# Kernel tuning notes

Hardware: AMD Instinct MI355X
Metric: run time of the kernel (lower is better)

## Reference

```python
import jax, jax.numpy as jnp
import numpy as np

NK, NV, DK, DV = 16, 32, 128, 128
R = NV // NK
KCONV, CHUNK = 4, 64
KEY_DIM, VALUE_DIM = NK * DK, NV * DV
CONV_DIM = 2 * KEY_DIM + VALUE_DIM
HIDDEN = 2048
B, S = 1, 4096


def _l2norm(x, eps=1e-6):
    return x * jax.lax.rsqrt(jnp.sum(x * x, -1, keepdims=True) + eps)


def _causal_dwconv(x, w):
    # x: [B, C, S], w: [C, K]; depthwise causal conv (pad K-1 on left),
    # equivalent to torch F.conv1d(groups=C, padding=K-1)[..., :S]
    K = w.shape[-1]
    T = x.shape[-1]
    xp = jnp.pad(x, ((0, 0), (0, 0), (K - 1, 0)))
    out = jnp.zeros_like(x)
    for j in range(K):  # fixed tiny kernel taps
        out = out + w[None, :, j, None] * xp[:, :, j:j + T]
    return out


def _chunk_gated_delta_rule(q, k, v, g, beta):
    # q,k: [B,S,H,DK], v: [B,S,H,DV], g,beta: [B,S,H]; S % CHUNK == 0
    dtype0 = q.dtype
    q = _l2norm(q)
    k = _l2norm(k)
    tr = lambda x: jnp.swapaxes(x, 1, 2).astype(jnp.float32)
    q, k, v = tr(q), tr(k), tr(v)
    g = jnp.swapaxes(g, 1, 2).astype(jnp.float32)
    beta = jnp.swapaxes(beta, 1, 2).astype(jnp.float32)
    Bb, H, T, dk = k.shape
    dv = v.shape[-1]
    N = T // CHUNK
    q = q * dk ** -0.5
    v_beta = v * beta[..., None]
    k_beta = k * beta[..., None]
    resh = lambda x: x.reshape(Bb, H, N, CHUNK, x.shape[-1])
    q, k, v, k_beta, v_beta = map(resh, (q, k, v, k_beta, v_beta))
    g = jnp.cumsum(g.reshape(Bb, H, N, CHUNK), axis=-1)
    lo = jnp.tril(jnp.ones((CHUNK, CHUNK), bool))
    lo_strict = jnp.tril(jnp.ones((CHUNK, CHUNK), bool), -1)
    gdiff = g[..., :, None] - g[..., None, :]
    decay = jnp.where(lo, jnp.exp(jnp.where(lo, gdiff, 0.0)), 0.0)  # [B,H,N,C,C]
    # strictly-lower M = tril_{-1}(k_beta @ k^T * decay); the original in-chunk
    # forward-substitution loop computes exactly (I + M)^{-1}
    M = jnp.where(lo_strict, jnp.einsum('bhnik,bhnjk->bhnij', k_beta, k) * decay, 0.0)
    eye = jnp.eye(CHUNK, dtype=jnp.float32)
    T_inv = jax.scipy.linalg.solve_triangular(
        eye + M, jnp.broadcast_to(eye, M.shape), lower=True, unit_diagonal=True)
    v_c = jnp.einsum('bhnij,bhnjv->bhniv', T_inv, v_beta)
    k_cumdecay = jnp.einsum('bhnij,bhnjk->bhnik', T_inv, k_beta * jnp.exp(g)[..., None])
    attn_local = jnp.where(lo, jnp.einsum('bhnik,bhnjk->bhnij', q, k) * decay, 0.0)
    mv = lambda x: jnp.moveaxis(x, 2, 0)  # chunk axis to front for scan
    xs = (mv(q), mv(k), mv(v_c), mv(g), mv(attn_local), mv(k_cumdecay))
    S0 = jnp.zeros((Bb, H, dk, dv), jnp.float32)

    def step(state, inp):
        q_i, k_i, v_i, g_i, attn_i, kcd_i = inp
        g_last = g_i[..., -1]  # [B,H]
        v_prime = jnp.einsum('bhik,bhkv->bhiv', kcd_i, state)
        v_new = v_i - v_prime
        attn_inter = jnp.einsum('bhik,bhkv->bhiv', q_i * jnp.exp(g_i)[..., None], state)
        out_i = attn_inter + jnp.einsum('bhij,bhjv->bhiv', attn_i, v_new)
        k_dec = k_i * jnp.exp(g_last[..., None] - g_i)[..., None]
        new_state = state * jnp.exp(g_last)[..., None, None] + \
            jnp.einsum('bhik,bhiv->bhkv', k_dec, v_new)
        return new_state, out_i

    _, outs = jax.lax.scan(step, S0, xs)  # [N,B,H,C,DV]
    core = jnp.moveaxis(outs, 0, 2).reshape(Bb, H, T, dv)
    return jnp.swapaxes(core, 1, 2).astype(dtype0)


def _forward(hidden_states, W_qkvz, W_ba, conv_w, dt_bias, A_log, norm_weight, W_out):
    Bx, Sx, _ = hidden_states.shape
    qkvz = (hidden_states @ W_qkvz).reshape(Bx, Sx, NK, 2 * DK + 2 * R * DV)
    ba = (hidden_states @ W_ba).reshape(Bx, Sx, NK, 2 * R)
    q = qkvz[..., :DK]
    k = qkvz[..., DK:2 * DK]
    v = qkvz[..., 2 * DK:2 * DK + R * DV].reshape(Bx, Sx, NV, DV)
    z = qkvz[..., 2 * DK + R * DV:].reshape(Bx, Sx, NV, DV)
    b = ba[..., :R].reshape(Bx, Sx, NV)
    a = ba[..., R:].reshape(Bx, Sx, NV)
    mixed = jnp.concatenate(
        [q.reshape(Bx, Sx, -1), k.reshape(Bx, Sx, -1), v.reshape(Bx, Sx, -1)], axis=-1)
    mixed = jax.nn.silu(_causal_dwconv(jnp.swapaxes(mixed, 1, 2), conv_w))
    mixed = jnp.swapaxes(mixed, 1, 2)
    q = mixed[..., :KEY_DIM].reshape(Bx, Sx, NK, DK)
    k = mixed[..., KEY_DIM:2 * KEY_DIM].reshape(Bx, Sx, NK, DK)
    v = mixed[..., 2 * KEY_DIM:].reshape(Bx, Sx, NV, DV)
    beta = jax.nn.sigmoid(b)
    g = -jnp.exp(A_log.astype(jnp.float32)) * jax.nn.softplus(
        a.astype(jnp.float32) + dt_bias.astype(jnp.float32))
    q = jnp.repeat(q, R, axis=2)  # GQA: expand k-heads to v-heads
    k = jnp.repeat(k, R, axis=2)
    core = _chunk_gated_delta_rule(q, k, v, g, beta)  # [B,S,NV,DV]
    h = core.astype(jnp.float32)
    h = h * jax.lax.rsqrt(jnp.mean(h * h, axis=-1, keepdims=True) + 1e-6)
    h = norm_weight * h
    h = h * jax.nn.silu(z.astype(jnp.float32))
    return h.reshape(Bx, Sx, VALUE_DIM) @ W_out


def setup_inputs() -> dict:
    ks = jax.random.split(jax.random.key(0), 8)
    return {
        'hidden_states': jax.random.normal(ks[0], (B, S, HIDDEN), jnp.float32),
        'W_qkvz': jax.random.normal(ks[1], (HIDDEN, 2 * KEY_DIM + 2 * VALUE_DIM), jnp.float32) * 0.02,
        'W_ba': jax.random.normal(ks[2], (HIDDEN, 2 * NV), jnp.float32) * 0.02,
        'conv_w': jax.random.normal(ks[3], (CONV_DIM, KCONV), jnp.float32) * 0.2,
        'dt_bias': jax.random.normal(ks[4], (NV,), jnp.float32) * 0.1,
        'A_log': jax.random.normal(ks[5], (NV,), jnp.float32) * 0.1,
        'norm_weight': jnp.ones((DV,), jnp.float32),
        'W_out': jax.random.normal(ks[6], (VALUE_DIM, HIDDEN), jnp.float32) * 0.02,
    }


def reference(hidden_states, W_qkvz, W_ba, conv_w, dt_bias, A_log, norm_weight, W_out):
    return _forward(hidden_states, W_qkvz, W_ba, conv_w, dt_bias, A_log, norm_weight, W_out)
```

## Files before the change

kernel.cpp:

```cpp
#include <hip/hip_runtime.h>

typedef unsigned short u16;
typedef __attribute__((ext_vector_type(2))) float f32x2;
typedef __attribute__((ext_vector_type(4))) float f32x4;
typedef __attribute__((ext_vector_type(2))) u16 u16x2;
typedef __attribute__((ext_vector_type(4))) u16 u16x4;
typedef __attribute__((ext_vector_type(8))) u16 u16x8;
typedef __attribute__((ext_vector_type(8))) __bf16 bf16x8;

__device__ __forceinline__ float bf2f(u16 u){ unsigned v = ((unsigned)u) << 16; return __builtin_bit_cast(float, v); }
__device__ __forceinline__ u16 f2bf(float f){
  unsigned u = __builtin_bit_cast(unsigned, f);
  u += 0x7fffu + ((u >> 16) & 1u);
  return (u16)(u >> 16);
}
__device__ __forceinline__ f32x4 b4f(u16x4 u){
  f32x4 r; r[0] = bf2f(u[0]); r[1] = bf2f(u[1]); r[2] = bf2f(u[2]); r[3] = bf2f(u[3]); return r;
}
__device__ __forceinline__ u16x4 p4(f32x4 v){
  u16x4 o; o[0] = f2bf(v[0]); o[1] = f2bf(v[1]); o[2] = f2bf(v[2]); o[3] = f2bf(v[3]); return o;
}
__device__ __forceinline__ void gld16(const void* g, const void* l){
  __builtin_amdgcn_global_load_lds((__attribute__((address_space(1))) void*)(void*)g,
                                   (__attribute__((address_space(3))) void*)(void*)l, 16, 0, 0);
}
__device__ __forceinline__ float sigmoidf(float x){ return 1.f / (1.f + expf(-x)); }
__device__ __forceinline__ float siluf(float x){ return x / (1.f + expf(-x)); }

#define GBAR() do { asm volatile("" ::: "memory"); __builtin_amdgcn_s_barrier(); asm volatile("" ::: "memory"); } while(0)

__global__ __launch_bounds__(256) void k_cast(const float* __restrict__ in, u16* __restrict__ out, int n4){
  int t = blockIdx.x * 256 + threadIdx.x;
  if (t >= n4) return;
  f32x4 v = ((const f32x4*)in)[t];
  u16x4 o;
  o[0] = f2bf(v[0]); o[1] = f2bf(v[1]); o[2] = f2bf(v[2]); o[3] = f2bf(v[3]);
  ((u16x4*)out)[t] = o;
}

template<int PERM>
__global__ __launch_bounds__(256) void k_trans(const float* __restrict__ in, u16* __restrict__ out, int K, int N){
  __shared__ float tile[32][33];
  int tx = threadIdx.x, ty = threadIdx.y;
  int n0 = blockIdx.x * 32, k0 = blockIdx.y * 32;
  #pragma unroll
  for (int j = 0; j < 32; j += 8) tile[ty + j][tx] = in[(size_t)(k0 + ty + j) * N + n0 + tx];
  __syncthreads();
  #pragma unroll
  for (int j = 0; j < 32; j += 8){
    int n = n0 + ty + j;
    int np;
    if (PERM){
      int g = n / 768, r = n - g * 768;
      np = (r < 512) ? (g * 512 + r) : (8192 + g * 256 + (r - 512));
    } else np = n;
    out[(size_t)np * K + k0 + tx] = f2bf(tile[tx][ty + j]);
  }
}

template<int MODE>
__global__ __launch_bounds__(512) void k_gemm256(const u16* __restrict__ A, const u16* __restrict__ Bt,
                                                 void* __restrict__ C, void* __restrict__ C2, int N, int K){
  __shared__ alignas(16) char lds[131072];
  const int tid = threadIdx.x;
  const int wid = tid >> 6, lane = tid & 63;
  const int vl = lane & 15, kg = lane >> 4;
  const int wm = wid >> 2, wn = wid & 3;
  const int nwg = (int)gridDim.x;
  const int swzb = ((int)blockIdx.x & 7) * (nwg >> 3) + ((int)blockIdx.x >> 3);
  const int nbx = N >> 8;
  const int bx = swzb % nbx, by = swzb / nbx;
  const int gm = by << 8, gn = bx << 8;
  const int nt = K >> 6;

  auto stageA = [&](int t, int h){
    if (t >= nt) return;
    const int k0 = t << 6;
    char* slot = lds + ((t & 1) * 2 + h) * 16384;
    #pragma unroll
    for (int p = 0; p < 2; p++){
      int o = p * 8192 + wid * 1024 + lane * 16;
      int sr = o >> 7, cs = (o >> 4) & 7;
      int gr = gm + ((sr >> 6) << 7) + h * 64 + (sr & 63);
      int gc = k0 + ((cs ^ (sr & 7)) << 3);
      gld16(A + (size_t)gr * K + gc, slot + p * 8192 + wid * 1024);
    }
  };
  auto stageB = [&](int t, int h){
    if (t >= nt) return;
    const int k0 = t << 6;
    char* slot = lds + 65536 + ((t & 1) * 2 + h) * 16384;
    #pragma unroll
    for (int p = 0; p < 2; p++){
      int o = p * 8192 + wid * 1024 + lane * 16;
      int sr = o >> 7, cs = (o >> 4) & 7;
      int gr = gn + ((sr >> 5) << 6) + h * 32 + (sr & 31);
      int gc = k0 + ((cs ^ (sr & 7)) << 3);
      gld16(Bt + (size_t)gr * K + gc, slot + p * 8192 + wid * 1024);
    }
  };

  f32x4 acc[8][4];
  #pragma unroll
  for (int a = 0; a < 8; a++)
    #pragma unroll
    for (int b = 0; b < 4; b++) acc[a][b] = 0.f;

  stageA(0, 0); stageB(0, 0); stageA(0, 1); stageB(0, 1); stageA(1, 0); stageB(1, 0);
  asm volatile("s_waitcnt vmcnt(8)" ::: "memory");
  GBAR();

#define PHASE(MH, NH, STAGECALL, VMSEL) do { \
    const char* Asl_ = lds + ((cur * 2 + (MH)) * 16384); \
    const char* Bsl_ = lds + 65536 + ((cur * 2 + (NH)) * 16384); \
    bf16x8 af_[4][2], bf_[2][2]; \
    _Pragma("unroll") \
    for (int mi = 0; mi < 4; mi++){ \
      int sr = wm * 64 + mi * 16 + vl; \
      _Pragma("unroll") \
      for (int ks = 0; ks < 2; ks++) \
        af_[mi][ks] = __builtin_bit_cast(bf16x8, *(const u16x8*)(Asl_ + sr * 128 + (((ks * 4 + kg) ^ (vl & 7)) << 4))); \
    } \
    _Pragma("unroll") \
    for (int ni = 0; ni < 2; ni++){ \
      int br = wn * 32 + ni * 16 + vl; \
      _Pragma("unroll") \
      for (int ks = 0; ks < 2; ks++) \
        bf_[ni][ks] = __builtin_bit_cast(bf16x8, *(const u16x8*)(Bsl_ + br * 128 + (((ks * 4 + kg) ^ (vl & 7)) << 4))); \
    } \
    STAGECALL; \
    __builtin_amdgcn_s_setprio(1); \
    _Pragma("unroll") \
    for (int mi = 0; mi < 4; mi++) \
      _Pragma("unroll") \
      for (int ni = 0; ni < 2; ni++) \
        _Pragma("unroll") \
        for (int ks = 0; ks < 2; ks++) \
          acc[(MH) * 4 + mi][(NH) * 2 + ni] = __builtin_amdgcn_mfma_f32_16x16x32_bf16(af_[mi][ks], bf_[ni][ks], acc[(MH) * 4 + mi][(NH) * 2 + ni], 0, 0, 0); \
    __builtin_amdgcn_s_setprio(0); \
    VMSEL; \
    GBAR(); \
  } while (0)

  for (int t = 0; t < nt; t++){
    const int cur = t & 1;
    const bool tail = (t >= nt - 3);
    PHASE(0, 0, stageA(t + 1, 1),
          { if (!tail) asm volatile("s_waitcnt vmcnt(6)" ::: "memory");
            else       asm volatile("s_waitcnt vmcnt(0)" ::: "memory"); });
    PHASE(0, 1, stageB(t + 1, 1), {});
    PHASE(1, 0, stageA(t + 2, 0), {});
    PHASE(1, 1, stageB(t + 2, 0),
          { if (!tail) asm volatile("s_waitcnt vmcnt(8)" ::: "memory");
            else       asm volatile("s_waitcnt vmcnt(0)" ::: "memory"); });
  }
#undef PHASE

  #pragma unroll
  for (int a = 0; a < 8; a++){
    int row = gm + wm * 128 + (a >> 2) * 64 + (a & 3) * 16 + (lane >> 4) * 4;
    #pragma unroll
    for (int b = 0; b < 4; b++){
      int col = gn + wn * 64 + (b >> 1) * 32 + (b & 1) * 16 + vl;
      #pragma unroll
      for (int j = 0; j < 4; j++){
        if (MODE == 0){
          ((float*)C)[(size_t)(row + j) * N + col] = acc[a][b][j];
        } else {
          if (col < 8192) ((u16*)C)[(size_t)(row + j) * 8192 + col]         = f2bf(acc[a][b][j]);
          else            ((u16*)C2)[(size_t)(row + j) * 4096 + col - 8192] = f2bf(acc[a][b][j]);
        }
      }
    }
  }
}

template<int MODE>
__global__ __launch_bounds__(256) void k_gemm(const u16* __restrict__ A, const u16* __restrict__ Bt,
                                              void* __restrict__ C, void* __restrict__ C2, int N, int K){
  __shared__ u16 As[128 * 32];
  __shared__ u16 Bs[128 * 32];
  const int tid = threadIdx.x;
  const int wave = tid >> 6, lane = tid & 63;
  const int nbx = (int)gridDim.x;
  const int nwg = nbx * (int)gridDim.y;
  const int linear = (int)blockIdx.y * nbx + (int)blockIdx.x;
  const int swz = (linear & 7) * (nwg >> 3) + (linear >> 3);
  const int gm = (swz / nbx) * 128, gn = (swz % nbx) * 128;
  const int c0 = wave * 2, c1 = c0 + 1;
  const int r0 = c0 * 16 + (lane >> 2), r1 = r0 + 16;
  const int kp = (lane & 3) * 8;
  const u16* a0 = A + (size_t)(gm + r0) * K + kp;
  const u16* a1 = A + (size_t)(gm + r1) * K + kp;
  const u16* b0 = Bt + (size_t)(gn + r0) * K + kp;
  const u16* b1 = Bt + (size_t)(gn + r1) * K + kp;
  const int wr = (wave >> 1) * 64, wc = (wave & 1) * 64;
  f32x4 acc[4][4];
  #pragma unroll
  for (int m = 0; m < 4; m++)
    #pragma unroll
    for (int n = 0; n < 4; n++) acc[m][n] = 0.f;
  for (int k0 = 0; k0 < K; k0 += 32){
    __syncthreads();
    gld16(a0 + k0, &As[c0 * 512]);
    gld16(a1 + k0, &As[c1 * 512]);
    gld16(b0 + k0, &Bs[c0 * 512]);
    gld16(b1 + k0, &Bs[c1 * 512]);
    __syncthreads();
    bf16x8 af[4], bfv[4];
    #pragma unroll
    for (int m = 0; m < 4; m++)
      af[m] = __builtin_bit_cast(bf16x8, *(const u16x8*)&As[(wr + m * 16 + (lane & 15)) * 32 + (lane >> 4) * 8]);
    #pragma unroll
    for (int n = 0; n < 4; n++)
      bfv[n] = __builtin_bit_cast(bf16x8, *(const u16x8*)&Bs[(wc + n * 16 + (lane & 15)) * 32 + (lane >> 4) * 8]);
    #pragma unroll
    for (int m = 0; m < 4; m++)
      #pragma unroll
      for (int n = 0; n < 4; n++)
        acc[m][n] = __builtin_amdgcn_mfma_f32_16x16x32_bf16(af[m], bfv[n], acc[m][n], 0, 0, 0);
  }
  #pragma unroll
  for (int m = 0; m < 4; m++){
    int row = gm + wr + m * 16 + (lane >> 4) * 4;
    #pragma unroll
    for (int n = 0; n < 4; n++){
      int col = gn + wc + n * 16 + (lane & 15);
      #pragma unroll
      for (int j = 0; j < 4; j++){
        if (MODE == 0){
          ((float*)C)[(size_t)(row + j) * N + col] = acc[m][n][j];
        } else {
          if (col < 8192) ((u16*)C)[(size_t)(row + j) * 8192 + col]         = f2bf(acc[m][n][j]);
          else            ((u16*)C2)[(size_t)(row + j) * 4096 + col - 8192] = f2bf(acc[m][n][j]);
        }
      }
    }
  }
}

__global__ __launch_bounds__(256) void k_ba(const float* __restrict__ hs, const float* __restrict__ Wba,
                                            float* __restrict__ ba){
  int wave = threadIdx.x >> 6, lane = threadIdx.x & 63;
  int s0 = (blockIdx.x * 4 + wave) * 4;
  f32x4 acc = 0.f;
  for (int k = 0; k < 2048; k += 4){
    float w0 = Wba[(size_t)(k + 0) * 64 + lane];
    float w1 = Wba[(size_t)(k + 1) * 64 + lane];
    float w2 = Wba[(size_t)(k + 2) * 64 + lane];
    float w3 = Wba[(size_t)(k + 3) * 64 + lane];
    f32x4 h0 = *(const f32x4*)&hs[(size_t)(s0 + 0) * 2048 + k];
    f32x4 h1 = *(const f32x4*)&hs[(size_t)(s0 + 1) * 2048 + k];
    f32x4 h2 = *(const f32x4*)&hs[(size_t)(s0 + 2) * 2048 + k];
    f32x4 h3 = *(const f32x4*)&hs[(size_t)(s0 + 3) * 2048 + k];
    acc[0] += h0[0]*w0 + h0[1]*w1 + h0[2]*w2 + h0[3]*w3;
    acc[1] += h1[0]*w0 + h1[1]*w1 + h1[2]*w2 + h1[3]*w3;
    acc[2] += h2[0]*w0 + h2[1]*w1 + h2[2]*w2 + h2[3]*w3;
    acc[3] += h3[0]*w0 + h3[1]*w1 + h3[2]*w2 + h3[3]*w3;
  }
  #pragma unroll
  for (int r = 0; r < 4; r++) ba[(size_t)(s0 + r) * 64 + lane] = acc[r];
}

__global__ __launch_bounds__(256) void k_conv(const u16* __restrict__ qkvB, const float* __restrict__ cw,
                                              float* __restrict__ qcF, float* __restrict__ kcF, u16* __restrict__ vcB){
  int idx = blockIdx.x * 256 + threadIdx.x;
  int c8 = idx & 1023, s = idx >> 10;
  int c = c8 * 8;
  int col;
  if (c < 2048)      { int hh = c >> 7, d = c & 127; col = hh * 512 + d; }
  else if (c < 4096) { int cc = c - 2048, hh = cc >> 7, d = cc & 127; col = hh * 512 + 128 + d; }
  else               { int cc = c - 4096, nv = cc >> 7, d = cc & 127; col = (nv >> 1) * 512 + 256 + (nv & 1) * 128 + d; }
  float w[8][4];
  #pragma unroll
  for (int e = 0; e < 8; e++){
    f32x4 wv = *(const f32x4*)&cw[(size_t)(c + e) * 4];
    #pragma unroll
    for (int j = 0; j < 4; j++) w[e][j] = wv[j];
  }
  float acc[8] = {0.f,0.f,0.f,0.f,0.f,0.f,0.f,0.f};
  #pragma unroll
  for (int j = 0; j < 4; j++){
    int sp = s - 3 + j;
    if (sp < 0) continue;
    u16x8 x = *(const u16x8*)&qkvB[(size_t)sp * 8192 + col];
    #pragma unroll
    for (int e = 0; e < 8; e++) acc[e] += w[e][j] * bf2f(x[e]);
  }
  if (c < 4096){
    float* outp = (c < 2048) ? qcF + (size_t)s * 2048 + c : kcF + (size_t)s * 2048 + (c - 2048);
    f32x4 oa, ob;
    #pragma unroll
    for (int e = 0; e < 4; e++) oa[e] = siluf(acc[e]);
    #pragma unroll
    for (int e = 0; e < 4; e++) ob[e] = siluf(acc[e + 4]);
    *(f32x4*)&outp[0] = oa;
    *(f32x4*)&outp[4] = ob;
  } else {
    u16x8 ov;
    #pragma unroll
    for (int e = 0; e < 8; e++) ov[e] = f2bf(siluf(acc[e]));
    *(u16x8*)&vcB[(size_t)s * 4096 + (c - 4096)] = ov;
  }
}

__global__ __launch_bounds__(256) void k_bg(const float* __restrict__ ba, const float* __restrict__ Alog,
                                            const float* __restrict__ dtb, float* __restrict__ betaO,
                                            float* __restrict__ gO){
  int idx = blockIdx.x * 256 + threadIdx.x;
  int s = idx >> 5, nv = idx & 31;
  float b = ba[(size_t)s * 64 + (nv >> 1) * 4 + (nv & 1)];
  float a = ba[(size_t)s * 64 + (nv >> 1) * 4 + 2 + (nv & 1)];
  betaO[idx] = sigmoidf(b);
  float x = a + dtb[nv];
  float sp = (x > 20.f) ? x : log1pf(expf(x));
  gO[idx] = -expf(Alog[nv]) * sp;
}

__global__ __launch_bounds__(256) void k_rownorm(const float* __restrict__ qcF, const float* __restrict__ kcF,
                                                 u16* __restrict__ qcB, u16* __restrict__ kcB){
  int wave = threadIdx.x >> 6, lane = threadIdx.x & 63;
  int row = blockIdx.x * 4 + wave;
  const float* src = (row < 65536) ? qcF + (size_t)row * 128 : kcF + (size_t)(row - 65536) * 128;
  u16* dst = (row < 65536) ? qcB + (size_t)row * 128 : kcB + (size_t)(row - 65536) * 128;
  float sc = (row < 65536) ? 0.08838834764831845f : 1.f;
  f32x2 v = ((const f32x2*)src)[lane];
  float ss = v[0] * v[0] + v[1] * v[1];
  #pragma unroll
  for (int off = 32; off; off >>= 1) ss += __shfl_xor(ss, off);
  float inv = rsqrtf(ss + 1e-6f) * sc;
  u16x2 o; o[0] = f2bf(v[0] * inv); o[1] = f2bf(v[1] * inv);
  ((u16x2*)dst)[lane] = o;
}

__global__ __launch_bounds__(256) void k_pre(const u16* __restrict__ qcB, const u16* __restrict__ kcB,
    const u16* __restrict__ vcB, const float* __restrict__ betaB, const float* __restrict__ gB,
    char* __restrict__ scanA, char* __restrict__ scanBg, u16* __restrict__ vcrG){
  __shared__ float sK[64 * 132];
  __shared__ float sX[64 * 264];
  __shared__ float sM[64 * 68];
  __shared__ float sG[64];
  __shared__ float sEg[64];
  __shared__ float sBeta[64];
  float* sQ = sX;
  const int tid = threadIdx.x;
  const int nv = blockIdx.x & 31, chunk = blockIdx.x >> 5;
  const int h = nv >> 1, s0 = chunk * 64;
  char* gA = scanA + ((size_t)nv * 64 + chunk) * 25600;
  u16* kcdG = (u16*)gA;
  u16* attnG = (u16*)(gA + 16384);
  float* egG = (float*)(gA + 24576);
  char* gB2 = scanBg + ((size_t)h * 64 + chunk) * 32768;
  u16* qG  = (u16*)gB2;
  u16* ktG = (u16*)(gB2 + 16384);
  if (tid < 64){
    float g = gB[(size_t)(s0 + tid) * 32 + nv];
    #pragma unroll
    for (int off = 1; off < 64; off <<= 1){ float nb = __shfl_up(g, off); if (tid >= off) g += nb; }
    sG[tid] = g;
    float g63 = __shfl(g, 63);
    float eg = expf(g);
    sEg[tid] = eg;
    egG[tid] = eg;
    egG[64 + tid] = expf(g63 - g);
  } else if (tid < 128){
    sBeta[tid - 64] = betaB[(size_t)(s0 + tid - 64) * 32 + nv];
  }
  for (int t = tid; t < 2048; t += 256){
    int i = t >> 5, d = (t & 31) * 4;
    *(f32x4*)&sK[i * 132 + d] = b4f(*(const u16x4*)&kcB[(size_t)(s0 + i) * 2048 + h * 128 + d]);
    *(f32x4*)&sQ[i * 132 + d] = b4f(*(const u16x4*)&qcB[(size_t)(s0 + i) * 2048 + h * 128 + d]);
  }
  __syncthreads();
  const int jb = tid & 15, ib = tid >> 4;
  float mA[4][4] = {}, aA[4][4] = {};
  for (int k = 0; k < 128; k += 4){
    f32x4 kA[4], qA[4], kB[4];
    #pragma unroll
    for (int r = 0; r < 4; r++){
      kA[r] = *(const f32x4*)&sK[(ib * 4 + r) * 132 + k];
      qA[r] = *(const f32x4*)&sQ[(ib * 4 + r) * 132 + k];
      kB[r] = *(const f32x4*)&sK[(jb * 4 + r) * 132 + k];
    }
    #pragma unroll
    for (int r = 0; r < 4; r++)
      #pragma unroll
      for (int c2 = 0; c2 < 4; c2++)
        #pragma unroll
        for (int kk = 0; kk < 4; kk++){
          mA[r][c2] += kA[r][kk] * kB[c2][kk];
          aA[r][c2] += qA[r][kk] * kB[c2][kk];
        }
  }
  #pragma unroll
  for (int r = 0; r < 4; r++){
    int i = ib * 4 + r;
    float gi = sG[i], bi = sBeta[i];
    f32x4 mrow;
    u16x4 arow;
    #pragma unroll
    for (int c2 = 0; c2 < 4; c2++){
      int j = jb * 4 + c2;
      float dec = expf(gi - sG[j]);
      mrow[c2] = (i > j)  ? mA[r][c2] * bi * dec : 0.f;
      arow[c2] = f2bf((i >= j) ? aA[r][c2] * dec : 0.f);
    }
    *(f32x4*)&sM[i * 68 + jb * 4] = mrow;
    *(u16x4*)&attnG[i * 64 + ((jb * 4) ^ ((i & 7) << 3))] = arow;
  }
  if (!(nv & 1)){
    for (int t = tid; t < 2048; t += 256){
      int i = t >> 5, d = (t & 31) * 4;
      f32x4 qv = *(const f32x4*)&sQ[i * 132 + d];
      u16x4 o; o[0]=f2bf(qv[0]); o[1]=f2bf(qv[1]); o[2]=f2bf(qv[2]); o[3]=f2bf(qv[3]);
      *(u16x4*)&qG[i * 128 + (d ^ ((i & 7) << 3))] = o;
    }
    for (int t = tid; t < 2048; t += 256){
      int k = t & 127, i0 = (t >> 7) * 4;
      u16x4 o;
      #pragma unroll
      for (int r = 0; r < 4; r++) o[r] = f2bf(sK[(i0 + r) * 132 + k]);
      *(u16x4*)&ktG[k * 64 + (i0 ^ ((k & 7) << 3))] = o;
    }
  }
  __syncthreads();
  for (int t = tid; t < 2048; t += 256){
    int i = t >> 5, d = (t & 31) * 4;
    float bi = sBeta[i];
    f32x4 v = b4f(*(const u16x4*)&vcB[(size_t)(s0 + i) * 4096 + nv * 128 + d]);
    v *= bi;
    *(f32x4*)&sX[i * 264 + d] = v;
    f32x4 kb = *(const f32x4*)&sK[i * 132 + d];
    kb *= bi * sEg[i];
    *(f32x4*)&sX[i * 264 + 128 + d] = kb;
  }
  __syncthreads();
  float x[64];
  #pragma unroll
  for (int i = 0; i < 64; i++) x[i] = sX[i * 264 + tid];
  #pragma unroll
  for (int i = 1; i < 64; i++){
    #pragma unroll
    for (int j = 0; j < i; j++) x[i] -= sM[i * 68 + j] * x[j];
  }
  #pragma unroll
  for (int i = 0; i < 64; i++) sX[i * 264 + tid] = x[i];
  __syncthreads();
  for (int t = tid; t < 2048; t += 256){
    int i = t >> 5, d = (t & 31) * 4;
    u16x4 b; b[0]=f2bf(sX[i*264+128+d]); b[1]=f2bf(sX[i*264+128+d+1]); b[2]=f2bf(sX[i*264+128+d+2]); b[3]=f2bf(sX[i*264+128+d+3]);
    *(u16x4*)&kcdG[i * 128 + (d ^ ((i & 7) << 3))] = b;
  }
  u16* vcrBlk = vcrG + ((size_t)nv * 64 + chunk) * 8192;
  for (int t = tid; t < 2048; t += 256){
    int vcol = t >> 4, m = (t >> 2) & 3, r = t & 3;
    int i0 = m * 16 + r * 4;
    u16x4 a;
    #pragma unroll
    for (int j = 0; j < 4; j++) a[j] = f2bf(sX[(i0 + j) * 264 + vcol]);
    *(u16x4*)&vcrBlk[(((m * 8 + (vcol >> 4)) * 64) + r * 16 + (vcol & 15)) * 4] = a;
  }
}

__device__ __forceinline__ void scan_chunk(
    const char* CURB, char* OTHB, u16x4* VCUR, u16x4* VOTH, int CH,
    const char* scanA, const char* scanBg, const u16* vcrG, u16* coreB,
    u16* sST, u16* sVnT, u16* sVeT, f32x4* S,
    int nv, int h, int vg, int wave, int lane, int vgrp, int myv, int swv){
  const int vl = lane & 15, kg = lane >> 4;
  if (CH + 1 < 64){
    const char* gA = scanA + ((size_t)nv * 64 + CH + 1) * 25600;
    for (int slot = wave; slot < 25; slot += 4)
      gld16(gA + slot * 1024 + lane * 16, OTHB + slot * 1024);
    const char* gB2 = scanBg + ((size_t)h * 64 + CH + 1) * 32768;
    for (int slot = wave; slot < 32; slot += 4)
      gld16(gB2 + slot * 1024 + lane * 16, OTHB + 25600 + slot * 1024);
    const u16* vc = vcrG + ((size_t)nv * 64 + CH + 1) * 8192;
    #pragma unroll
    for (int m = 0; m < 4; m++)
      VOTH[m] = *(const u16x4*)&vc[((m * 8 + vgrp) * 64 + lane) * 4];
  }
  const u16* kcdL  = (const u16*)(CURB);
  const u16* attnL = (const u16*)(CURB + 16384);
  const float* egL = (const float*)(CURB + 24576);
  const u16* qL    = (const u16*)(CURB + 25600);
  const u16* ktL   = (const u16*)(CURB + 25600 + 16384);
  f32x4 vp[4], ai[4];
  #pragma unroll
  for (int m = 0; m < 4; m++){ vp[m] = 0.f; ai[m] = 0.f; }
  #pragma unroll
  for (int kt = 0; kt < 4; kt++){
    int ko = kt * 32 + kg * 8;
    bf16x8 sf = __builtin_bit_cast(bf16x8, *(const u16x8*)&sST[myv * 128 + (ko ^ swv)]);
    #pragma unroll
    for (int m = 0; m < 4; m++){
      int row = m * 16 + vl, rs = (row & 7) << 3;
      bf16x8 kf = __builtin_bit_cast(bf16x8, *(const u16x8*)&kcdL[row * 128 + (ko ^ rs)]);
      vp[m] = __builtin_amdgcn_mfma_f32_16x16x32_bf16(kf, sf, vp[m], 0, 0, 0);
      bf16x8 qf = __builtin_bit_cast(bf16x8, *(const u16x8*)&qL[row * 128 + (ko ^ rs)]);
      ai[m] = __builtin_amdgcn_mfma_f32_16x16x32_bf16(qf, sf, ai[m], 0, 0, 0);
    }
  }
  float eL = egL[63];
  #pragma unroll
  for (int m = 0; m < 4; m++){
    f32x4 vn = b4f(VCUR[m]) - vp[m];
    f32x4 ed4 = *(const f32x4*)&egL[64 + m * 16 + kg * 4];
    f32x4 eg4 = *(const f32x4*)&egL[m * 16 + kg * 4];
    int ja = (m * 16 + kg * 4) ^ swv;
    *(u16x4*)&sVnT[myv * 64 + ja] = p4(vn);
    *(u16x4*)&sVeT[myv * 64 + ja] = p4(vn * ed4);
    ai[m] *= eg4;
  }
  #pragma unroll
  for (int ms = 0; ms < 8; ms++) S[ms] *= eL;
  #pragma unroll
  for (int jt = 0; jt < 2; jt++){
    int jo = jt * 32 + kg * 8;
    bf16x8 vnf = __builtin_bit_cast(bf16x8, *(const u16x8*)&sVnT[myv * 64 + (jo ^ swv)]);
    bf16x8 vef = __builtin_bit_cast(bf16x8, *(const u16x8*)&sVeT[myv * 64 + (jo ^ swv)]);
    #pragma unroll
    for (int m = 0; m < 4; m++){
      int row = m * 16 + vl, rs = (row & 7) << 3;
      bf16x8 af = __builtin_bit_cast(bf16x8, *(const u16x8*)&attnL[row * 64 + (jo ^ rs)]);
      ai[m] = __builtin_amdgcn_mfma_f32_16x16x32_bf16(af, vnf, ai[m], 0, 0, 0);
    }
    #pragma unroll
    for (int ms = 0; ms < 8; ms++){
      int krow = ms * 16 + vl, rs = (krow & 7) << 3;
      bf16x8 kf = __builtin_bit_cast(bf16x8, *(const u16x8*)&ktL[krow * 64 + (jo ^ rs)]);
      S[ms] = __builtin_amdgcn_mfma_f32_16x16x32_bf16(kf, vef, S[ms], 0, 0, 0);
    }
  }
  #pragma unroll
  for (int m = 0; m < 4; m++){
    size_t ig = (size_t)CH * 64 + m * 16 + kg * 4;
    size_t base = (ig * 32 + nv) * 128 + vg * 64 + wave * 16 + vl;
    #pragma unroll
    for (int j = 0; j < 4; j++) coreB[base + (size_t)j * 4096] = f2bf(ai[m][j]);
  }
  #pragma unroll
  for (int ms = 0; ms < 8; ms++){
    int k0 = ms * 16 + kg * 4;
    *(u16x4*)&sST[myv * 128 + (k0 ^ swv)] = p4(S[ms]);
  }
  __syncthreads();
}

__global__ __launch_bounds__(256) void k_scan(const char* __restrict__ scanA, const char* __restrict__ scanBg,
    const u16* __restrict__ vcrG, u16* __restrict__ coreB){
  __shared__ alignas(16) char sbuf[2 * 58368];
  __shared__ alignas(16) u16 sST[64 * 128];
  __shared__ alignas(16) u16 sVnT[64 * 64];
  __shared__ alignas(16) u16 sVeT[64 * 64];
  const int tid = threadIdx.x;
  const int wave = tid >> 6, lane = tid & 63;
  const int nv = blockIdx.x & 31, vg = blockIdx.x >> 5;
  const int h = nv >> 1;
  const int vgrp = vg * 4 + wave;
  const int myv = wave * 16 + (lane & 15);
  const int swv = (myv & 7) << 3;
  for (int t = tid; t < 8192; t += 256) sST[t] = 0;
  f32x4 S[8];
  #pragma unroll
  for (int ms = 0; ms < 8; ms++) S[ms] = 0.f;
  u16x4 vA[4], vB[4];
  {
    const char* gA = scanA + (size_t)(nv * 64) * 25600;
    for (int slot = wave; slot < 25; slot += 4)
      gld16(gA + slot * 1024 + lane * 16, sbuf + slot * 1024);
    const char* gB2 = scanBg + (size_t)(h * 64) * 32768;
    for (int slot = wave; slot < 32; slot += 4)
      gld16(gB2 + slot * 1024 + lane * 16, sbuf + 25600 + slot * 1024);
    const u16* vc = vcrG + (size_t)(nv * 64) * 8192;
    #pragma unroll
    for (int m = 0; m < 4; m++)
      vA[m] = *(const u16x4*)&vc[((m * 8 + vgrp) * 64 + lane) * 4];
  }
  __syncthreads();
  for (int c = 0; c < 64; c += 2){
    scan_chunk(sbuf,         sbuf + 58368, vA, vB, c,
               scanA, scanBg, vcrG, coreB, sST, sVnT, sVeT, S,
               nv, h, vg, wave, lane, vgrp, myv, swv);
    scan_chunk(sbuf + 58368, sbuf,         vB, vA, c + 1,
               scanA, scanBg, vcrG, coreB, sST, sVnT, sVeT, S,
               nv, h, vg, wave, lane, vgrp, myv, swv);
  }
}

__global__ __launch_bounds__(256) void k_gate(const u16* __restrict__ coreB, const u16* __restrict__ zB,
                                              const float* __restrict__ nw, u16* __restrict__ hb){
  int wave = threadIdx.x >> 6, lane = threadIdx.x & 63;
  int row = blockIdx.x * 4 + wave;
  int s = row >> 5, nv = row & 31;
  u16x2 cu = *(const u16x2*)&coreB[(size_t)row * 128 + lane * 2];
  float c0 = bf2f(cu[0]), c1 = bf2f(cu[1]);
  float ss = c0 * c0 + c1 * c1;
  #pragma unroll
  for (int off = 32; off; off >>= 1) ss += __shfl_xor(ss, off);
  float rms = rsqrtf(ss * (1.f / 128.f) + 1e-6f);
  int zcol = (nv >> 1) * 256 + (nv & 1) * 128 + lane * 2;
  u16x2 zu = *(const u16x2*)&zB[(size_t)s * 4096 + zcol];
  float z0 = siluf(bf2f(zu[0])), z1 = siluf(bf2f(zu[1]));
  u16x2 ho;
  ho[0] = f2bf(c0 * rms * nw[lane * 2]     * z0);
  ho[1] = f2bf(c1 * rms * nw[lane * 2 + 1] * z1);
  *(u16x2*)&hb[(size_t)row * 128 + lane * 2] = ho;
}

extern "C" void kernel_launch(void* const* d_in, const int* in_sizes, int n_in,
                              void* d_out, int out_size, void* d_ws, size_t ws_size,
                              hipStream_t stream){
  (void)in_sizes; (void)n_in; (void)out_size; (void)ws_size;
  const float* hs    = (const float*)d_in[0];
  const float* Wqkvz = (const float*)d_in[1];
  const float* Wba   = (const float*)d_in[2];
  const float* cw    = (const float*)d_in[3];
  const float* dtb   = (const float*)d_in[4];
  const float* Alog  = (const float*)d_in[5];
  const float* nw    = (const float*)d_in[6];
  const float* Wout  = (const float*)d_in[7];
  char* ws = (char*)d_ws;
  const size_t MB = 1ull << 20;
  u16*   hsb   = (u16*)  (ws + 0);
  u16*   wqT   = (u16*)  (ws + 16 * MB);
  float* qcF   = (float*)(ws + 0);
  u16*   vcrG  = (u16*)  (ws + 0);
  u16*   hb    = (u16*)  (ws + 0);
  u16*   vcB   = (u16*)  (ws + 32 * MB);
  u16*   qkvB  = (u16*)  (ws + 64 * MB);
  char*  scanA =         (ws + 64 * MB);
  float* ba    = (float*)(ws + 114 * MB);
  float* betaB = (float*)(ws + 115 * MB);
  float* gB    = (float*)(ws + 115 * MB + 512 * 1024);
  u16*   zB    = (u16*)  (ws + 128 * MB);
  u16*   qcB   = (u16*)  (ws + 160 * MB);
  u16*   kcB   = (u16*)  (ws + 176 * MB);
  u16*   coreB = (u16*)  (ws + 160 * MB);
  float* kcF   = (float*)(ws + 192 * MB);
  char*  scanBg=         (ws + 192 * MB);
  u16*   woT   = (u16*)  (ws + 192 * MB);
  float* out   = (float*)d_out;

  k_cast<<<8192, 256, 0, stream>>>(hs, hsb, 2097152);
  k_trans<1><<<dim3(384, 64), dim3(32, 8), 0, stream>>>(Wqkvz, wqT, 2048, 12288);
  k_gemm256<2><<<768, 512, 0, stream>>>(hsb, wqT, qkvB, zB, 12288, 2048);
  k_conv<<<16384, 256, 0, stream>>>(qkvB, cw, qcF, kcF, vcB);
  k_ba<<<256, 256, 0, stream>>>(hs, Wba, ba);
  k_bg<<<512, 256, 0, stream>>>(ba, Alog, dtb, betaB, gB);
  k_rownorm<<<32768, 256, 0, stream>>>(qcF, kcF, qcB, kcB);
  k_pre<<<2048, 256, 0, stream>>>(qcB, kcB, vcB, betaB, gB, scanA, scanBg, vcrG);
  k_scan<<<64, 256, 0, stream>>>(scanA, scanBg, vcrG, coreB);
  k_gate<<<32768, 256, 0, stream>>>(coreB, zB, nw, hb);
  k_trans<0><<<dim3(64, 128), dim3(32, 8), 0, stream>>>(Wout, woT, 4096, 2048);
  k_gemm<0><<<dim3(16, 32), 256, 0, stream>>>(hb, woT, out, nullptr, 2048, 4096);
}
```

Baseline: 1.295 ms.

## Use MFMA for chunk K·K^T and Q·K^T, write swizzled bf16 q/k from rownorm

k_rownorm now writes normalized q straight into the scan buffer's swizzled layout and k into a per-chunk swizzled buffer, so k_pre no longer rebuilds q. k_pre loads these bf16 tiles into LDS with direct global-to-LDS loads and computes the K·Kᵀ and Q·Kᵀ chunk products with bf16 MFMA instead of scalar fp32 FMAs. The triangular solve now keeps its right-hand sides in registers, reading v from global and k from LDS, and writes outputs directly from registers, which removes the fp32 staging buffer and a couple of barriers. The cost is bf16-precision inputs to these products and more scattered global stores in rownorm.

```diff
diff --git a/kernel.cpp b/kernel.cpp
--- a/kernel.cpp
+++ b/kernel.cpp
@@ -318,32 +318,36 @@
 }
 
 __global__ __launch_bounds__(256) void k_rownorm(const float* __restrict__ qcF, const float* __restrict__ kcF,
-                                                 u16* __restrict__ qcB, u16* __restrict__ kcB){
+                                                 char* __restrict__ scanBg, u16* __restrict__ kSwz){
   int wave = threadIdx.x >> 6, lane = threadIdx.x & 63;
   int row = blockIdx.x * 4 + wave;
-  const float* src = (row < 65536) ? qcF + (size_t)row * 128 : kcF + (size_t)(row - 65536) * 128;
-  u16* dst = (row < 65536) ? qcB + (size_t)row * 128 : kcB + (size_t)(row - 65536) * 128;
-  float sc = (row < 65536) ? 0.08838834764831845f : 1.f;
+  bool isq = row < 65536;
+  int r = isq ? row : row - 65536;
+  const float* src = (isq ? qcF : kcF) + (size_t)r * 128;
+  int s = r >> 4, h = r & 15;
+  int chunk = s >> 6, i = s & 63;
+  float sc = isq ? 0.08838834764831845f : 1.f;
   f32x2 v = ((const f32x2*)src)[lane];
   float ss = v[0] * v[0] + v[1] * v[1];
   #pragma unroll
   for (int off = 32; off; off >>= 1) ss += __shfl_xor(ss, off);
   float inv = rsqrtf(ss + 1e-6f) * sc;
   u16x2 o; o[0] = f2bf(v[0] * inv); o[1] = f2bf(v[1] * inv);
-  ((u16x2*)dst)[lane] = o;
-}
-
-__global__ __launch_bounds__(256) void k_pre(const u16* __restrict__ qcB, const u16* __restrict__ kcB,
-    const u16* __restrict__ vcB, const float* __restrict__ betaB, const float* __restrict__ gB,
+  int col = (lane * 2) ^ ((i & 7) << 3);
+  if (isq) *(u16x2*)(scanBg + ((size_t)(h * 64 + chunk)) * 32768 + (size_t)(i * 128 + col) * 2) = o;
+  else     *(u16x2*)&kSwz[((size_t)(h * 64 + chunk)) * 8192 + i * 128 + col] = o;
+}
+
+__global__ __launch_bounds__(256) void k_pre(const u16* __restrict__ kSwz, const u16* __restrict__ vcB,
+    const float* __restrict__ betaB, const float* __restrict__ gB,
     char* __restrict__ scanA, char* __restrict__ scanBg, u16* __restrict__ vcrG){
-  __shared__ float sK[64 * 132];
-  __shared__ float sX[64 * 264];
+  __shared__ alignas(16) u16 sKb[8192];
+  __shared__ alignas(16) u16 sQb[8192];
   __shared__ float sM[64 * 68];
   __shared__ float sG[64];
   __shared__ float sEg[64];
   __shared__ float sBeta[64];
-  float* sQ = sX;
-  const int tid = threadIdx.x;
+  const int tid = threadIdx.x, wave = tid >> 6, lane = tid & 63;
   const int nv = blockIdx.x & 31, chunk = blockIdx.x >> 5;
   const int h = nv >> 1, s0 = chunk * 64;
   char* gA = scanA + ((size_t)nv * 64 + chunk) * 25600;
@@ -351,114 +355,102 @@
   u16* attnG = (u16*)(gA + 16384);
   float* egG = (float*)(gA + 24576);
   char* gB2 = scanBg + ((size_t)h * 64 + chunk) * 32768;
-  u16* qG  = (u16*)gB2;
   u16* ktG = (u16*)(gB2 + 16384);
+  const char* kblk = (const char*)(kSwz + ((size_t)h * 64 + chunk) * 8192);
+  const char* qblk = (const char*)gB2;
+  for (int t = wave; t < 16; t += 4){
+    gld16(kblk + t * 1024 + lane * 16, (char*)sKb + t * 1024);
+    gld16(qblk + t * 1024 + lane * 16, (char*)sQb + t * 1024);
+  }
   if (tid < 64){
     float g = gB[(size_t)(s0 + tid) * 32 + nv];
     #pragma unroll
     for (int off = 1; off < 64; off <<= 1){ float nb = __shfl_up(g, off); if (tid >= off) g += nb; }
-    sG[tid] = g;
     float g63 = __shfl(g, 63);
     float eg = expf(g);
-    sEg[tid] = eg;
-    egG[tid] = eg;
-    egG[64 + tid] = expf(g63 - g);
+    sG[tid] = g; sEg[tid] = eg;
+    egG[tid] = eg; egG[64 + tid] = expf(g63 - g);
   } else if (tid < 128){
     sBeta[tid - 64] = betaB[(size_t)(s0 + tid - 64) * 32 + nv];
   }
-  for (int t = tid; t < 2048; t += 256){
-    int i = t >> 5, d = (t & 31) * 4;
-    *(f32x4*)&sK[i * 132 + d] = b4f(*(const u16x4*)&kcB[(size_t)(s0 + i) * 2048 + h * 128 + d]);
-    *(f32x4*)&sQ[i * 132 + d] = b4f(*(const u16x4*)&qcB[(size_t)(s0 + i) * 2048 + h * 128 + d]);
-  }
   __syncthreads();
-  const int jb = tid & 15, ib = tid >> 4;
-  float mA[4][4] = {}, aA[4][4] = {};
-  for (int k = 0; k < 128; k += 4){
-    f32x4 kA[4], qA[4], kB[4];
-    #pragma unroll
-    for (int r = 0; r < 4; r++){
-      kA[r] = *(const f32x4*)&sK[(ib * 4 + r) * 132 + k];
-      qA[r] = *(const f32x4*)&sQ[(ib * 4 + r) * 132 + k];
-      kB[r] = *(const f32x4*)&sK[(jb * 4 + r) * 132 + k];
-    }
-    #pragma unroll
-    for (int r = 0; r < 4; r++)
+  const int vl = lane & 15, kg = lane >> 4;
+  f32x4 Mf[4], Af[4];
+  #pragma unroll
+  for (int m = 0; m < 4; m++){ Mf[m] = 0.f; Af[m] = 0.f; }
+  const int brow = wave * 16 + vl;
+  const int bs = (brow & 7) << 3;
+  #pragma unroll
+  for (int kt = 0; kt < 4; kt++){
+    int ko = kt * 32 + kg * 8;
+    bf16x8 bk = __builtin_bit_cast(bf16x8, *(const u16x8*)&sKb[brow * 128 + (ko ^ bs)]);
+    #pragma unroll
+    for (int m = 0; m < 4; m++){
+      int ar = m * 16 + vl, as = (ar & 7) << 3;
+      bf16x8 ak = __builtin_bit_cast(bf16x8, *(const u16x8*)&sKb[ar * 128 + (ko ^ as)]);
+      Mf[m] = __builtin_amdgcn_mfma_f32_16x16x32_bf16(ak, bk, Mf[m], 0, 0, 0);
+      bf16x8 aq = __builtin_bit_cast(bf16x8, *(const u16x8*)&sQb[ar * 128 + (ko ^ as)]);
+      Af[m] = __builtin_amdgcn_mfma_f32_16x16x32_bf16(aq, bk, Af[m], 0, 0, 0);
+    }
+  }
+  {
+    const int j = wave * 16 + vl;
+    float gj = sG[j];
+    #pragma unroll
+    for (int m = 0; m < 4; m++){
       #pragma unroll
-      for (int c2 = 0; c2 < 4; c2++)
-        #pragma unroll
-        for (int kk = 0; kk < 4; kk++){
-          mA[r][c2] += kA[r][kk] * kB[c2][kk];
-          aA[r][c2] += qA[r][kk] * kB[c2][kk];
-        }
-  }
-  #pragma unroll
-  for (int r = 0; r < 4; r++){
-    int i = ib * 4 + r;
-    float gi = sG[i], bi = sBeta[i];
-    f32x4 mrow;
-    u16x4 arow;
-    #pragma unroll
-    for (int c2 = 0; c2 < 4; c2++){
-      int j = jb * 4 + c2;
-      float dec = expf(gi - sG[j]);
-      mrow[c2] = (i > j)  ? mA[r][c2] * bi * dec : 0.f;
-      arow[c2] = f2bf((i >= j) ? aA[r][c2] * dec : 0.f);
-    }
-    *(f32x4*)&sM[i * 68 + jb * 4] = mrow;
-    *(u16x4*)&attnG[i * 64 + ((jb * 4) ^ ((i & 7) << 3))] = arow;
+      for (int r = 0; r < 4; r++){
+        int i = m * 16 + kg * 4 + r;
+        float dec = expf(sG[i] - gj);
+        sM[i * 68 + j] = (i > j) ? Mf[m][r] * sBeta[i] * dec : 0.f;
+        attnG[i * 64 + (j ^ ((i & 7) << 3))] = f2bf((i >= j) ? Af[m][r] * dec : 0.f);
+      }
+    }
   }
   if (!(nv & 1)){
     for (int t = tid; t < 2048; t += 256){
-      int i = t >> 5, d = (t & 31) * 4;
-      f32x4 qv = *(const f32x4*)&sQ[i * 132 + d];
-      u16x4 o; o[0]=f2bf(qv[0]); o[1]=f2bf(qv[1]); o[2]=f2bf(qv[2]); o[3]=f2bf(qv[3]);
-      *(u16x4*)&qG[i * 128 + (d ^ ((i & 7) << 3))] = o;
-    }
-    for (int t = tid; t < 2048; t += 256){
-      int k = t & 127, i0 = (t >> 7) * 4;
+      int k = t & 127, i0 = (t >> 7) << 2;
       u16x4 o;
       #pragma unroll
-      for (int r = 0; r < 4; r++) o[r] = f2bf(sK[(i0 + r) * 132 + k]);
+      for (int r2 = 0; r2 < 4; r2++)
+        o[r2] = sKb[(i0 + r2) * 128 + (k ^ (((i0 + r2) & 7) << 3))];
       *(u16x4*)&ktG[k * 64 + (i0 ^ ((k & 7) << 3))] = o;
     }
-  }
-  __syncthreads();
-  for (int t = tid; t < 2048; t += 256){
-    int i = t >> 5, d = (t & 31) * 4;
-    float bi = sBeta[i];
-    f32x4 v = b4f(*(const u16x4*)&vcB[(size_t)(s0 + i) * 4096 + nv * 128 + d]);
-    v *= bi;
-    *(f32x4*)&sX[i * 264 + d] = v;
-    f32x4 kb = *(const f32x4*)&sK[i * 132 + d];
-    kb *= bi * sEg[i];
-    *(f32x4*)&sX[i * 264 + 128 + d] = kb;
   }
   __syncthreads();
   float x[64];
-  #pragma unroll
-  for (int i = 0; i < 64; i++) x[i] = sX[i * 264 + tid];
+  if (tid < 128){
+    const u16* vp = vcB + (size_t)s0 * 4096 + (size_t)nv * 128 + tid;
+    #pragma unroll
+    for (int i = 0; i < 64; i++) x[i] = bf2f(vp[(size_t)i * 4096]) * sBeta[i];
+  } else {
+    int d = tid - 128;
+    #pragma unroll
+    for (int i = 0; i < 64; i++)
+      x[i] = bf2f(sKb[i * 128 + (d ^ ((i & 7) << 3))]) * sBeta[i] * sEg[i];
+  }
   #pragma unroll
   for (int i = 1; i < 64; i++){
     #pragma unroll
-    for (int j = 0; j < i; j++) x[i] -= sM[i * 68 + j] * x[j];
-  }
-  #pragma unroll
-  for (int i = 0; i < 64; i++) sX[i * 264 + tid] = x[i];
-  __syncthreads();
-  for (int t = tid; t < 2048; t += 256){
-    int i = t >> 5, d = (t & 31) * 4;
-    u16x4 b; b[0]=f2bf(sX[i*264+128+d]); b[1]=f2bf(sX[i*264+128+d+1]); b[2]=f2bf(sX[i*264+128+d+2]); b[3]=f2bf(sX[i*264+128+d+3]);
-    *(u16x4*)&kcdG[i * 128 + (d ^ ((i & 7) << 3))] = b;
-  }
-  u16* vcrBlk = vcrG + ((size_t)nv * 64 + chunk) * 8192;
-  for (int t = tid; t < 2048; t += 256){
-    int vcol = t >> 4, m = (t >> 2) & 3, r = t & 3;
-    int i0 = m * 16 + r * 4;
-    u16x4 a;
-    #pragma unroll
-    for (int j = 0; j < 4; j++) a[j] = f2bf(sX[(i0 + j) * 264 + vcol]);
-    *(u16x4*)&vcrBlk[(((m * 8 + (vcol >> 4)) * 64) + r * 16 + (vcol & 15)) * 4] = a;
+    for (int jj = 0; jj < i; jj++) x[i] -= sM[i * 68 + jj] * x[jj];
+  }
+  if (tid < 128){
+    u16* vb = vcrG + ((size_t)nv * 64 + chunk) * 8192;
+    int c = tid;
+    #pragma unroll
+    for (int m = 0; m < 4; m++)
+      #pragma unroll
+      for (int r = 0; r < 4; r++){
+        u16x4 a;
+        #pragma unroll
+        for (int q2 = 0; q2 < 4; q2++) a[q2] = f2bf(x[m * 16 + r * 4 + q2]);
+        *(u16x4*)&vb[(((m * 8 + (c >> 4)) * 64) + r * 16 + (c & 15)) * 4] = a;
+      }
+  } else {
+    int d = tid - 128;
+    #pragma unroll
+    for (int i = 0; i < 64; i++)
+      kcdG[i * 128 + (d ^ ((i & 7) << 3))] = f2bf(x[i]);
   }
 }
 
@@ -634,12 +626,11 @@
   float* betaB = (float*)(ws + 115 * MB);
   float* gB    = (float*)(ws + 115 * MB + 512 * 1024);
   u16*   zB    = (u16*)  (ws + 128 * MB);
-  u16*   qcB   = (u16*)  (ws + 160 * MB);
-  u16*   kcB   = (u16*)  (ws + 176 * MB);
+  float* kcF   = (float*)(ws + 160 * MB);
   u16*   coreB = (u16*)  (ws + 160 * MB);
-  float* kcF   = (float*)(ws + 192 * MB);
   char*  scanBg=         (ws + 192 * MB);
   u16*   woT   = (u16*)  (ws + 192 * MB);
+  u16*   kSwz  = (u16*)  (ws + 224 * MB);
   float* out   = (float*)d_out;
 
   k_cast<<<8192, 256, 0, stream>>>(hs, hsb, 2097152);
@@ -648,8 +639,8 @@
   k_conv<<<16384, 256, 0, stream>>>(qkvB, cw, qcF, kcF, vcB);
   k_ba<<<256, 256, 0, stream>>>(hs, Wba, ba);
   k_bg<<<512, 256, 0, stream>>>(ba, Alog, dtb, betaB, gB);
-  k_rownorm<<<32768, 256, 0, stream>>>(qcF, kcF, qcB, kcB);
-  k_pre<<<2048, 256, 0, stream>>>(qcB, kcB, vcB, betaB, gB, scanA, scanBg, vcrG);
+  k_rownorm<<<32768, 256, 0, stream>>>(qcF, kcF, scanBg, kSwz);
+  k_pre<<<2048, 256, 0, stream>>>(kSwz, vcB, betaB, gB, scanA, scanBg, vcrG);
   k_scan<<<64, 256, 0, stream>>>(scanA, scanBg, vcrG, coreB);
   k_gate<<<32768, 256, 0, stream>>>(coreB, zB, nw, hb);
   k_trans<0><<<dim3(64, 128), dim3(32, 8), 0, stream>>>(Wout, woT, 4096, 2048);
```

New measurement: 1.148 ms. 11.3% less time.
